# Kernel optimization log

Hardware: AMD Instinct MI355X
Metric: run time of the kernel (lower is better)

## Reference

```python
import jax, jax.numpy as jnp
import numpy as np

N_EMBD = 768
N_HEAD = 12
N_KV_HEAD = 4                      # repeat factor in _repeat_kv
NUM_KV_HEADS = N_HEAD // N_KV_HEAD # 3 actual kv heads
HEAD_DIM = N_EMBD // N_HEAD        # 64
BLOCK_SIZE = 1024                  # sliding window size
SCALE = (HEAD_DIM * N_KV_HEAD / N_HEAD) ** (-0.5)


def _rotary_cos_sin(T, d, dtype):
    inv_freq = 1.0 / (10000.0 ** (jnp.arange(0, d, 2, dtype=jnp.float32) / d))
    t = jnp.arange(T, dtype=jnp.float32)
    freqs = jnp.outer(t, inv_freq)  # (T, d/2)
    return jnp.cos(freqs).astype(dtype)[None, None], jnp.sin(freqs).astype(dtype)[None, None]


def _apply_rotary(x):
    # x: (b, h, T, d)
    T, d = x.shape[2], x.shape[3]
    cos, sin = _rotary_cos_sin(T, d, x.dtype)
    x1, x2 = x[..., : d // 2], x[..., d // 2 :]
    return jnp.concatenate([x1 * cos - x2 * sin, x1 * sin + x2 * cos], axis=-1)


def setup_inputs() -> dict:
    key = jax.random.key(0)
    k0, k1, k2, k3, k4 = jax.random.split(key, 5)
    b, T = 2, 2048
    s = 0.02
    return {
        "hidden_states": jax.random.normal(k0, (b, T, N_EMBD), jnp.float32),
        "Wq": jax.random.normal(k1, (N_HEAD * HEAD_DIM, N_EMBD), jnp.float32) * s,
        "Wk": jax.random.normal(k2, (NUM_KV_HEADS * HEAD_DIM, N_EMBD), jnp.float32) * s,
        "Wv": jax.random.normal(k3, (NUM_KV_HEADS * HEAD_DIM, N_EMBD), jnp.float32) * s,
        "Wo": jax.random.normal(k4, (N_EMBD, N_HEAD * HEAD_DIM), jnp.float32) * s,
    }


def reference(hidden_states, Wq, Wk, Wv, Wo):
    b, T, _ = hidden_states.shape
    q = (hidden_states @ Wq.T).reshape(b, T, N_HEAD, HEAD_DIM).transpose(0, 2, 1, 3)
    k = (hidden_states @ Wk.T).reshape(b, T, NUM_KV_HEADS, HEAD_DIM).transpose(0, 2, 1, 3)
    v = (hidden_states @ Wv.T).reshape(b, T, NUM_KV_HEADS, HEAD_DIM).transpose(0, 2, 1, 3)

    # _repeat_kv: each kv head repeated n_kv_head (=4) times contiguously
    k = jnp.repeat(k, N_KV_HEAD, axis=1)
    v = jnp.repeat(v, N_KV_HEAD, axis=1)

    q = _apply_rotary(q)
    k = _apply_rotary(k)

    # centered sliding-window mask (faithful to per-token loop):
    # window_start = clip(i - W//2, 0, T - W); window is always exactly W wide
    W = BLOCK_SIZE
    i = jnp.arange(T)[:, None]
    j = jnp.arange(T)[None, :]
    start = jnp.clip(i - W // 2, 0, T - W)
    mask = (j >= start) & (j < start + W)  # (T, T)

    scores = jnp.einsum("bhqd,bhkd->bhqk", q, k) * SCALE
    scores = jnp.where(mask[None, None], scores, jnp.finfo(scores.dtype).min)
    attn = jax.nn.softmax(scores, axis=-1)
    out = jnp.einsum("bhqk,bhkd->bhqd", attn, v)  # (b, h, T, d)

    out = out.transpose(0, 2, 1, 3).reshape(b, T, N_EMBD)
    return out @ Wo.T
```

## Files before the change

kernel.cpp:

```cpp
#include <hip/hip_runtime.h>
#include <math.h>

#define T_SEQ 2048
#define E 768
#define WIN 1024
#define KDIM 768
#define HS_SZ ((size_t)4096 * 768)
#define SCALE 0.21650635094610965f

typedef _Float16 f16x8 __attribute__((ext_vector_type(8)));
typedef _Float16 f16x4 __attribute__((ext_vector_type(4)));
typedef float f32x4 __attribute__((ext_vector_type(4)));
typedef __attribute__((address_space(3))) _Float16 lf16;

#define MFMA16(a, b, c) __builtin_amdgcn_mfma_f32_16x16x32_f16(a, b, c, 0, 0, 0)

__device__ __forceinline__ void dma16(const _Float16* g, lf16* l) {
    __builtin_amdgcn_global_load_lds(
        (const __attribute__((address_space(1))) void*)g,
        (__attribute__((address_space(3))) void*)l, 16, 0, 0);
}

__device__ __forceinline__ void cast8(const float* __restrict__ src,
                                      _Float16* __restrict__ dst, int i) {
    float4 a = *(const float4*)&src[i];
    float4 b = *(const float4*)&src[i + 4];
    f16x8 h;
    h[0] = (_Float16)a.x; h[1] = (_Float16)a.y; h[2] = (_Float16)a.z; h[3] = (_Float16)a.w;
    h[4] = (_Float16)b.x; h[5] = (_Float16)b.y; h[6] = (_Float16)b.z; h[7] = (_Float16)b.w;
    *(f16x8*)&dst[i] = h;
}

__global__ __launch_bounds__(256) void prep(
    const float* __restrict__ hs,
    const float* __restrict__ Wq, const float* __restrict__ Wk,
    const float* __restrict__ Wv, const float* __restrict__ Wo,
    _Float16* __restrict__ hs16,
    _Float16* __restrict__ Wq16, _Float16* __restrict__ Wk16,
    _Float16* __restrict__ Wv16, _Float16* __restrict__ Wo16,
    float2* __restrict__ rtab) {
    int tid = blockIdx.x * 256 + threadIdx.x;
    int i = tid * 8;
    if (i < 768 * 768) { cast8(Wq, Wq16, i); cast8(Wo, Wo16, i); }
    if (i < 192 * 768) { cast8(Wk, Wk16, i); cast8(Wv, Wv16, i); }
    cast8(hs, hs16, i);
    if (tid < 2048 * 32) {
        int t = tid >> 5, d = tid & 31;
        float inv = powf(10000.0f, -(float)(2 * d) * (1.0f / 64.0f));
        float s, c;
        sincosf((float)t * inv, &s, &c);
        rtab[tid] = make_float2(c, s);
    }
}

__global__ __launch_bounds__(256) void gemm_qkv(
    const _Float16* __restrict__ A16,
    const _Float16* __restrict__ Wq16, const _Float16* __restrict__ Wk16,
    const _Float16* __restrict__ Wv16, const float2* __restrict__ rtab,
    _Float16* __restrict__ q16, _Float16* __restrict__ k16,
    _Float16* __restrict__ vT16) {
    __shared__ __align__(16) _Float16 As[128 * 128];
    __shared__ __align__(16) _Float16 Bs[64 * 128];
    const int tid = threadIdx.x;
    const int bx = blockIdx.x;
    const int m0 = blockIdx.y * 128;
    const int w = tid >> 6, lane = tid & 63;
    const int mm = lane & 15, quad = lane >> 4;

    const _Float16* bbase; int brb;
    if (bx < 12)      { bbase = Wq16; brb = bx * 64; }
    else if (bx < 15) { bbase = Wk16; brb = (bx - 12) * 64; }
    else              { bbase = Wv16; brb = (bx - 15) * 64; }

    const int rofs4 = lane >> 4;
    const int gs = lane & 15;

    const _Float16* agp[8]; lf16* alp[8];
    #pragma unroll
    for (int j = 0; j < 8; ++j) {
        int c = j * 4 + w;
        int rr = c * 4 + rofs4;
        int glog = gs ^ (rr & 15);
        agp[j] = A16 + (size_t)(m0 + rr) * KDIM + glog * 8;
        alp[j] = ((lf16*)As) + c * 512 + lane * 8;
    }
    const _Float16* bgp[4]; lf16* blp[4];
    #pragma unroll
    for (int j = 0; j < 4; ++j) {
        int c = j * 4 + w;
        int rr = c * 4 + rofs4;
        int glog = gs ^ (rr & 15);
        bgp[j] = bbase + (size_t)(brb + rr) * KDIM + glog * 8;
        blp[j] = ((lf16*)Bs) + c * 512 + lane * 8;
    }

    f32x4 acc[2][4] = {};

    for (int it = 0; it < 6; ++it) {
        const int ke = it * 128;
        __syncthreads();
        #pragma unroll
        for (int j = 0; j < 8; ++j) dma16(agp[j] + ke, alp[j]);
        #pragma unroll
        for (int j = 0; j < 4; ++j) dma16(bgp[j] + ke, blp[j]);
        __syncthreads();
        #pragma unroll
        for (int s = 0; s < 4; ++s) {
            const int gq = ((s * 4 + quad) ^ mm) * 8;
            f16x8 ah[2];
            #pragma unroll
            for (int mt = 0; mt < 2; ++mt)
                ah[mt] = *(const f16x8*)&As[(w * 32 + mt * 16 + mm) * 128 + gq];
            #pragma unroll
            for (int nt = 0; nt < 4; ++nt) {
                f16x8 bh = *(const f16x8*)&Bs[(nt * 16 + mm) * 128 + gq];
                #pragma unroll
                for (int mt = 0; mt < 2; ++mt)
                    acc[mt][nt] = MFMA16(ah[mt], bh, acc[mt][nt]);
            }
        }
    }

    #pragma unroll
    for (int mt = 0; mt < 2; ++mt) {
        #pragma unroll
        for (int r = 0; r < 4; ++r) {
            int row = m0 + w * 32 + mt * 16 + quad * 4 + r;
            int t = row & (T_SEQ - 1);
            int b = row >> 11;
            if (bx < 12) {
                _Float16* dst = &q16[(size_t)row * E + bx * 64 + mm];
                #pragma unroll
                for (int nt = 0; nt < 2; ++nt) {
                    int d = nt * 16 + mm;
                    float2 cs = rtab[t * 32 + d];
                    float x1 = acc[mt][nt][r], x2 = acc[mt][nt + 2][r];
                    dst[nt * 16]       = (_Float16)((x1 * cs.x - x2 * cs.y) * SCALE);
                    dst[(nt + 2) * 16] = (_Float16)((x1 * cs.y + x2 * cs.x) * SCALE);
                }
            } else if (bx < 15) {
                int kvh = bx - 12;
                _Float16* dst = &k16[(((size_t)(b * 3 + kvh)) * T_SEQ + t) * 64 + mm];
                #pragma unroll
                for (int nt = 0; nt < 2; ++nt) {
                    int d = nt * 16 + mm;
                    float2 cs = rtab[t * 32 + d];
                    float x1 = acc[mt][nt][r], x2 = acc[mt][nt + 2][r];
                    dst[nt * 16]       = (_Float16)(x1 * cs.x - x2 * cs.y);
                    dst[(nt + 2) * 16] = (_Float16)(x1 * cs.y + x2 * cs.x);
                }
            } else {
                int kvh = bx - 15;
                #pragma unroll
                for (int nt = 0; nt < 4; ++nt) {
                    int d = nt * 16 + mm;
                    vT16[(((size_t)(b * 3 + kvh)) * 64 + d) * T_SEQ + t] = (_Float16)acc[mt][nt][r];
                }
            }
        }
    }
}

__global__ __launch_bounds__(256) void gemm_out(
    const _Float16* __restrict__ A16, const _Float16* __restrict__ B16,
    float* __restrict__ C) {
    __shared__ __align__(16) _Float16 As[64 * 128];
    __shared__ __align__(16) _Float16 Bs[64 * 128];
    const int tid = threadIdx.x;
    const int n0 = blockIdx.x * 64;
    const int m0 = blockIdx.y * 64;
    const int w = tid >> 6, lane = tid & 63;
    const int mm = lane & 15, quad = lane >> 4;
    const int wm = (w & 1) * 32, wn = (w >> 1) * 32;

    const int rofs4 = lane >> 4;
    const int gs = lane & 15;

    const _Float16* agp[4]; lf16* alp[4];
    const _Float16* bgp[4]; lf16* blp[4];
    #pragma unroll
    for (int j = 0; j < 4; ++j) {
        int c = j * 4 + w;
        int rr = c * 4 + rofs4;
        int glog = gs ^ (rr & 15);
        agp[j] = A16 + (size_t)(m0 + rr) * KDIM + glog * 8;
        alp[j] = ((lf16*)As) + c * 512 + lane * 8;
        bgp[j] = B16 + (size_t)(n0 + rr) * KDIM + glog * 8;
        blp[j] = ((lf16*)Bs) + c * 512 + lane * 8;
    }

    f32x4 acc[2][2] = {};

    for (int it = 0; it < 6; ++it) {
        const int ke = it * 128;
        __syncthreads();
        #pragma unroll
        for (int j = 0; j < 4; ++j) dma16(agp[j] + ke, alp[j]);
        #pragma unroll
        for (int j = 0; j < 4; ++j) dma16(bgp[j] + ke, blp[j]);
        __syncthreads();
        #pragma unroll
        for (int s = 0; s < 4; ++s) {
            const int gq = ((s * 4 + quad) ^ mm) * 8;
            f16x8 ah[2], bh[2];
            #pragma unroll
            for (int mt = 0; mt < 2; ++mt)
                ah[mt] = *(const f16x8*)&As[(wm + mt * 16 + mm) * 128 + gq];
            #pragma unroll
            for (int nt = 0; nt < 2; ++nt)
                bh[nt] = *(const f16x8*)&Bs[(wn + nt * 16 + mm) * 128 + gq];
            #pragma unroll
            for (int nt = 0; nt < 2; ++nt)
                #pragma unroll
                for (int mt = 0; mt < 2; ++mt)
                    acc[mt][nt] = MFMA16(ah[mt], bh[nt], acc[mt][nt]);
        }
    }
    #pragma unroll
    for (int mt = 0; mt < 2; ++mt)
        #pragma unroll
        for (int r = 0; r < 4; ++r) {
            int row = m0 + wm + mt * 16 + quad * 4 + r;
            float* cp = &C[(size_t)row * 768 + n0 + wn + mm];
            #pragma unroll
            for (int nt = 0; nt < 2; ++nt)
                cp[nt * 16] = acc[mt][nt][r];
        }
}

__global__ __launch_bounds__(256) void attn_mfma(const _Float16* __restrict__ q16,
                                                 const _Float16* __restrict__ k16,
                                                 const _Float16* __restrict__ vT16,
                                                 _Float16* __restrict__ aout16) {
    __shared__ __align__(16) char smem[8192 + 8192 + 10240];
    _Float16* k_s  = (_Float16*)smem;
    _Float16* vT_s = (_Float16*)(smem + 8192);
    _Float16 (*p_s)[40] = (_Float16(*)[40])(smem + 16384);
    float* ored = (float*)smem;
    float* lred = (float*)(smem + 16384);

    const int b = blockIdx.z, h = blockIdx.y;
    const int i0 = blockIdx.x * 64;
    const int plane = b * 3 + (h >> 2);
    const int tid = threadIdx.x;
    const int w = tid >> 6, lane = tid & 63;
    const int m = lane & 15, quad = lane >> 4;
    const int qh = w & 1, kh = w >> 1;
    const int xm = m & 7;

    int s0 = i0 - 512;      s0 = s0 < 0 ? 0 : (s0 > 1024 ? 1024 : s0);
    int sL = i0 + 63 - 512; sL = sL < 0 ? 0 : (sL > 1024 ? 1024 : sL);
    const int nc = (sL + WIN - s0 + 63) >> 6;

    int start_q[2];
    f16x8 qf[2][2];
    #pragma unroll
    for (int qt = 0; qt < 2; ++qt) {
        int qi = i0 + qh * 32 + qt * 16 + m;
        int sq = qi - 512; sq = sq < 0 ? 0 : (sq > 1024 ? 1024 : sq);
        start_q[qt] = sq;
        const _Float16* qp = &q16[((size_t)(b * T_SEQ + qi)) * E + h * 64 + quad * 8];
        qf[qt][0] = *(const f16x8*)&qp[0];
        qf[qt][1] = *(const f16x8*)&qp[32];
    }

    f32x4 o[2][4] = {};
    float l_run[2] = {0.0f, 0.0f};

    const int rofs = lane >> 3;
    const int glog = (lane & 7) ^ rofs;
    const _Float16* kgb[2]; const _Float16* vgb[2];
    _Float16* klw[2]; _Float16* vlw[2];
    #pragma unroll
    for (int j = 0; j < 2; ++j) {
        int rr = (j * 4 + w) * 8 + rofs;
        kgb[j] = k16 + ((size_t)plane * T_SEQ + rr) * 64 + glog * 8;
        vgb[j] = vT16 + ((size_t)plane * 64 + rr) * T_SEQ + glog * 8;
        klw[j] = k_s + (j * 4 + w) * 512 + lane * 8;
        vlw[j] = vT_s + (j * 4 + w) * 512 + lane * 8;
    }

    f16x8 kr[2], vr[2];
    #pragma unroll
    for (int j = 0; j < 2; ++j) {
        kr[j] = *(const f16x8*)(kgb[j] + (size_t)s0 * 64);
        vr[j] = *(const f16x8*)(vgb[j] + s0);
    }

    for (int ci = 0; ci < nc; ++ci) {
        const int c0 = s0 + ci * 64;
        __syncthreads();
        #pragma unroll
        for (int j = 0; j < 2; ++j) {
            *(f16x8*)klw[j] = kr[j];
            *(f16x8*)vlw[j] = vr[j];
        }
        __syncthreads();
        if (ci + 1 < nc) {
            const int cn = c0 + 64;
            #pragma unroll
            for (int j = 0; j < 2; ++j) {
                kr[j] = *(const f16x8*)(kgb[j] + (size_t)cn * 64);
                vr[j] = *(const f16x8*)(vgb[j] + cn);
            }
        }

        f32x4 st[2][2] = {};
        #pragma unroll
        for (int s = 0; s < 2; ++s) {
            #pragma unroll
            for (int kt = 0; kt < 2; ++kt) {
                int row = kh * 32 + kt * 16 + m;
                int g = (s * 4 + quad) ^ xm;
                f16x8 a = *(const f16x8*)&k_s[row * 64 + g * 8];
                #pragma unroll
                for (int qt = 0; qt < 2; ++qt)
                    st[kt][qt] = MFMA16(a, qf[qt][s], st[kt][qt]);
            }
        }

        const bool boundary = (c0 < sL) || (c0 + 63 > s0 + 1023);
        if (boundary) {
            #pragma unroll
            for (int kt = 0; kt < 2; ++kt)
                #pragma unroll
                for (int qt = 0; qt < 2; ++qt)
                    #pragma unroll
                    for (int r = 0; r < 4; ++r) {
                        int j = c0 + kh * 32 + kt * 16 + quad * 4 + r;
                        bool valid = (j >= start_q[qt]) && (j < start_q[qt] + WIN);
                        st[kt][qt][r] = valid ? st[kt][qt][r] : -INFINITY;
                    }
        }

        #pragma unroll
        for (int kt = 0; kt < 2; ++kt)
            #pragma unroll
            for (int qt = 0; qt < 2; ++qt) {
                float p0 = __expf(st[kt][qt][0]);
                float p1 = __expf(st[kt][qt][1]);
                float p2 = __expf(st[kt][qt][2]);
                float p3 = __expf(st[kt][qt][3]);
                l_run[qt] += (p0 + p1) + (p2 + p3);
                f16x4 pv = {(_Float16)p0, (_Float16)p1, (_Float16)p2, (_Float16)p3};
                *(f16x4*)&p_s[w * 32 + qt * 16 + m][kt * 16 + quad * 4] = pv;
            }

        f16x8 bp[2];
        #pragma unroll
        for (int qt = 0; qt < 2; ++qt)
            bp[qt] = *(const f16x8*)&p_s[w * 32 + qt * 16 + m][quad * 8];
        #pragma unroll
        for (int mt = 0; mt < 4; ++mt) {
            int g = (kh * 4 + quad) ^ xm;
            f16x8 a = *(const f16x8*)&vT_s[(mt * 16 + m) * 64 + g * 8];
            #pragma unroll
            for (int qt = 0; qt < 2; ++qt)
                o[qt][mt] = MFMA16(a, bp[qt], o[qt][mt]);
        }
    }

    float l_tot[2];
    #pragma unroll
    for (int qt = 0; qt < 2; ++qt) {
        float l = l_run[qt];
        l += __shfl_xor(l, 16);
        l += __shfl_xor(l, 32);
        l_tot[qt] = l;
    }

    __syncthreads();
    if (kh == 1) {
        #pragma unroll
        for (int qt = 0; qt < 2; ++qt) {
            #pragma unroll
            for (int mt = 0; mt < 4; ++mt) {
                int idx = ((qh * 32 + qt * 16 + m) << 6) + mt * 16 + quad * 4;
                *(float4*)&ored[idx] = *(float4*)&o[qt][mt];
            }
            if (quad == 0) lred[qh * 32 + qt * 16 + m] = l_tot[qt];
        }
    }
    __syncthreads();
    if (kh == 0) {
        #pragma unroll
        for (int qt = 0; qt < 2; ++qt) {
            float rl = 1.0f / (l_tot[qt] + lred[qh * 32 + qt * 16 + m]);
            int qi = i0 + qh * 32 + qt * 16 + m;
            _Float16* op = &aout16[((size_t)(b * T_SEQ + qi)) * E + h * 64];
            #pragma unroll
            for (int mt = 0; mt < 4; ++mt) {
                int idx = ((qh * 32 + qt * 16 + m) << 6) + mt * 16 + quad * 4;
                float4 other = *(float4*)&ored[idx];
                #pragma unroll
                for (int r = 0; r < 4; ++r) {
                    float x = (o[qt][mt][r] + (&other.x)[r]) * rl;
                    op[mt * 16 + quad * 4 + r] = (_Float16)x;
                }
            }
        }
    }
}

extern "C" void kernel_launch(void* const* d_in, const int* in_sizes, int n_in,
                              void* d_out, int out_size, void* d_ws, size_t ws_size,
                              hipStream_t stream) {
    const float* hs = (const float*)d_in[0];
    const float* Wq = (const float*)d_in[1];
    const float* Wk = (const float*)d_in[2];
    const float* Wv = (const float*)d_in[3];
    const float* Wo = (const float*)d_in[4];
    float* out = (float*)d_out;

    _Float16* hs16   = (_Float16*)d_ws;
    _Float16* aout16 = hs16 + HS_SZ;
    _Float16* q16    = aout16 + HS_SZ;
    _Float16* k16    = q16 + HS_SZ;
    _Float16* vT16   = k16 + 6 * 2048 * 64;
    _Float16* Wq16   = vT16 + 6 * 2048 * 64;
    _Float16* Wk16   = Wq16 + 768 * 768;
    _Float16* Wv16   = Wk16 + 192 * 768;
    _Float16* Wo16   = Wv16 + 192 * 768;
    float2*   rtab   = (float2*)(Wo16 + 768 * 768);

    dim3 blk(256);
    prep<<<dim3((int)(HS_SZ / 8 / 256)), blk, 0, stream>>>(hs, Wq, Wk, Wv, Wo,
                                                           hs16, Wq16, Wk16, Wv16, Wo16, rtab);
    gemm_qkv<<<dim3(18, 32), blk, 0, stream>>>(hs16, Wq16, Wk16, Wv16, rtab, q16, k16, vT16);
    attn_mfma<<<dim3(32, 12, 2), blk, 0, stream>>>(q16, k16, vT16, aout16);
    gemm_out<<<dim3(12, 64), blk, 0, stream>>>(aout16, Wo16, out);
}
```

Baseline: 135.2 us.

## Stage V transpose through LDS, double-buffer attention K/V, enlarge output GEMM tile

The V-projection epilogue now writes its tile into shared memory and emits coalesced 16-byte rows of vT, replacing scattered 2-byte strided stores. The attention kernel double-buffers its K/V shared tiles, which removes one barrier per chunk, and writes its output as 4-wide half vectors. The output GEMM uses 128-row tiles with a 4-wide N loop per wave, halving the grid for more reuse of the Wo tile. Costs are more shared memory in attention, which may lower occupancy, and fewer output GEMM blocks.

```diff
diff --git a/kernel.cpp b/kernel.cpp
--- a/kernel.cpp
+++ b/kernel.cpp
@@ -121,14 +121,13 @@
         }
     }
 
-    #pragma unroll
-    for (int mt = 0; mt < 2; ++mt) {
-        #pragma unroll
-        for (int r = 0; r < 4; ++r) {
-            int row = m0 + w * 32 + mt * 16 + quad * 4 + r;
-            int t = row & (T_SEQ - 1);
-            int b = row >> 11;
-            if (bx < 12) {
+    if (bx < 12) {
+        #pragma unroll
+        for (int mt = 0; mt < 2; ++mt)
+            #pragma unroll
+            for (int r = 0; r < 4; ++r) {
+                int row = m0 + w * 32 + mt * 16 + quad * 4 + r;
+                int t = row & (T_SEQ - 1);
                 _Float16* dst = &q16[(size_t)row * E + bx * 64 + mm];
                 #pragma unroll
                 for (int nt = 0; nt < 2; ++nt) {
@@ -138,8 +137,16 @@
                     dst[nt * 16]       = (_Float16)((x1 * cs.x - x2 * cs.y) * SCALE);
                     dst[(nt + 2) * 16] = (_Float16)((x1 * cs.y + x2 * cs.x) * SCALE);
                 }
-            } else if (bx < 15) {
-                int kvh = bx - 12;
+            }
+    } else if (bx < 15) {
+        int kvh = bx - 12;
+        #pragma unroll
+        for (int mt = 0; mt < 2; ++mt)
+            #pragma unroll
+            for (int r = 0; r < 4; ++r) {
+                int row = m0 + w * 32 + mt * 16 + quad * 4 + r;
+                int t = row & (T_SEQ - 1);
+                int b = row >> 11;
                 _Float16* dst = &k16[(((size_t)(b * 3 + kvh)) * T_SEQ + t) * 64 + mm];
                 #pragma unroll
                 for (int nt = 0; nt < 2; ++nt) {
@@ -149,14 +156,28 @@
                     dst[nt * 16]       = (_Float16)(x1 * cs.x - x2 * cs.y);
                     dst[(nt + 2) * 16] = (_Float16)(x1 * cs.y + x2 * cs.x);
                 }
-            } else {
-                int kvh = bx - 15;
-                #pragma unroll
-                for (int nt = 0; nt < 4; ++nt) {
-                    int d = nt * 16 + mm;
-                    vT16[(((size_t)(b * 3 + kvh)) * 64 + d) * T_SEQ + t] = (_Float16)acc[mt][nt][r];
-                }
-            }
+            }
+    } else {
+        __syncthreads();
+        _Float16 (*vs)[136] = (_Float16 (*)[136])As;
+        #pragma unroll
+        for (int mt = 0; mt < 2; ++mt)
+            #pragma unroll
+            for (int nt = 0; nt < 4; ++nt) {
+                f16x4 pv;
+                #pragma unroll
+                for (int r = 0; r < 4; ++r) pv[r] = (_Float16)acc[mt][nt][r];
+                *(f16x4*)&vs[nt * 16 + mm][w * 32 + mt * 16 + quad * 4] = pv;
+            }
+        __syncthreads();
+        const int kvh = bx - 15;
+        const int b = m0 >> 11, tbase = m0 & (T_SEQ - 1);
+        const int tl = (tid & 15) * 8;
+        #pragma unroll
+        for (int j = 0; j < 4; ++j) {
+            int dd = (tid >> 4) + j * 16;
+            f16x8 vv = *(const f16x8*)&vs[dd][tl];
+            *(f16x8*)&vT16[(((size_t)(b * 3 + kvh)) * 64 + dd) * T_SEQ + tbase + tl] = vv;
         }
     }
 }
@@ -164,66 +185,71 @@
 __global__ __launch_bounds__(256) void gemm_out(
     const _Float16* __restrict__ A16, const _Float16* __restrict__ B16,
     float* __restrict__ C) {
-    __shared__ __align__(16) _Float16 As[64 * 128];
+    __shared__ __align__(16) _Float16 As[128 * 128];
     __shared__ __align__(16) _Float16 Bs[64 * 128];
     const int tid = threadIdx.x;
     const int n0 = blockIdx.x * 64;
-    const int m0 = blockIdx.y * 64;
+    const int m0 = blockIdx.y * 128;
     const int w = tid >> 6, lane = tid & 63;
     const int mm = lane & 15, quad = lane >> 4;
-    const int wm = (w & 1) * 32, wn = (w >> 1) * 32;
 
     const int rofs4 = lane >> 4;
     const int gs = lane & 15;
 
-    const _Float16* agp[4]; lf16* alp[4];
-    const _Float16* bgp[4]; lf16* blp[4];
-    #pragma unroll
-    for (int j = 0; j < 4; ++j) {
+    const _Float16* agp[8]; lf16* alp[8];
+    #pragma unroll
+    for (int j = 0; j < 8; ++j) {
         int c = j * 4 + w;
         int rr = c * 4 + rofs4;
         int glog = gs ^ (rr & 15);
         agp[j] = A16 + (size_t)(m0 + rr) * KDIM + glog * 8;
         alp[j] = ((lf16*)As) + c * 512 + lane * 8;
+    }
+    const _Float16* bgp[4]; lf16* blp[4];
+    #pragma unroll
+    for (int j = 0; j < 4; ++j) {
+        int c = j * 4 + w;
+        int rr = c * 4 + rofs4;
+        int glog = gs ^ (rr & 15);
         bgp[j] = B16 + (size_t)(n0 + rr) * KDIM + glog * 8;
         blp[j] = ((lf16*)Bs) + c * 512 + lane * 8;
     }
 
-    f32x4 acc[2][2] = {};
+    f32x4 acc[2][4] = {};
 
     for (int it = 0; it < 6; ++it) {
         const int ke = it * 128;
         __syncthreads();
         #pragma unroll
-        for (int j = 0; j < 4; ++j) dma16(agp[j] + ke, alp[j]);
+        for (int j = 0; j < 8; ++j) dma16(agp[j] + ke, alp[j]);
         #pragma unroll
         for (int j = 0; j < 4; ++j) dma16(bgp[j] + ke, blp[j]);
         __syncthreads();
         #pragma unroll
         for (int s = 0; s < 4; ++s) {
             const int gq = ((s * 4 + quad) ^ mm) * 8;
-            f16x8 ah[2], bh[2];
+            f16x8 ah[2];
             #pragma unroll
             for (int mt = 0; mt < 2; ++mt)
-                ah[mt] = *(const f16x8*)&As[(wm + mt * 16 + mm) * 128 + gq];
-            #pragma unroll
-            for (int nt = 0; nt < 2; ++nt)
-                bh[nt] = *(const f16x8*)&Bs[(wn + nt * 16 + mm) * 128 + gq];
-            #pragma unroll
-            for (int nt = 0; nt < 2; ++nt)
+                ah[mt] = *(const f16x8*)&As[(w * 32 + mt * 16 + mm) * 128 + gq];
+            #pragma unroll
+            for (int nt = 0; nt < 4; ++nt) {
+                f16x8 bh = *(const f16x8*)&Bs[(nt * 16 + mm) * 128 + gq];
                 #pragma unroll
                 for (int mt = 0; mt < 2; ++mt)
-                    acc[mt][nt] = MFMA16(ah[mt], bh[nt], acc[mt][nt]);
-        }
-    }
+                    acc[mt][nt] = MFMA16(ah[mt], bh, acc[mt][nt]);
+            }
+        }
+    }
+
     #pragma unroll
     for (int mt = 0; mt < 2; ++mt)
         #pragma unroll
         for (int r = 0; r < 4; ++r) {
-            int row = m0 + wm + mt * 16 + quad * 4 + r;
-            float* cp = &C[(size_t)row * 768 + n0 + wn + mm];
-            #pragma unroll
-            for (int nt = 0; nt < 2; ++nt)
+            int row = m0 + w * 32 + mt * 16 + quad * 4 + r;
+            float* cp = &C[(size_t)row * 768 + n0 + mm];
+            #pragma unroll
+            for (int nt = 0; nt < 4; ++nt)
                 cp[nt * 16] = acc[mt][nt][r];
         }
 }
@@ -232,10 +258,10 @@
                                                  const _Float16* __restrict__ k16,
                                                  const _Float16* __restrict__ vT16,
                                                  _Float16* __restrict__ aout16) {
-    __shared__ __align__(16) char smem[8192 + 8192 + 10240];
+    __shared__ __align__(16) char smem[32768 + 10240];
     _Float16* k_s  = (_Float16*)smem;
-    _Float16* vT_s = (_Float16*)(smem + 8192);
-    _Float16 (*p_s)[40] = (_Float16(*)[40])(smem + 16384);
+    _Float16* vT_s = (_Float16*)(smem + 16384);
+    _Float16 (*p_s)[40] = (_Float16(*)[40])(smem + 32768);
     float* ored = (float*)smem;
     float* lred = (float*)(smem + 16384);
 
@@ -286,15 +312,15 @@
         kr[j] = *(const f16x8*)(kgb[j] + (size_t)s0 * 64);
         vr[j] = *(const f16x8*)(vgb[j] + s0);
     }
+    #pragma unroll
+    for (int j = 0; j < 2; ++j) {
+        *(f16x8*)klw[j] = kr[j];
+        *(f16x8*)vlw[j] = vr[j];
+    }
 
     for (int ci = 0; ci < nc; ++ci) {
         const int c0 = s0 + ci * 64;
-        __syncthreads();
-        #pragma unroll
-        for (int j = 0; j < 2; ++j) {
-            *(f16x8*)klw[j] = kr[j];
-            *(f16x8*)vlw[j] = vr[j];
-        }
+        const int sel = (ci & 1) * 4096;
         __syncthreads();
         if (ci + 1 < nc) {
             const int cn = c0 + 64;
@@ -312,7 +338,7 @@
             for (int kt = 0; kt < 2; ++kt) {
                 int row = kh * 32 + kt * 16 + m;
                 int g = (s * 4 + quad) ^ xm;
-                f16x8 a = *(const f16x8*)&k_s[row * 64 + g * 8];
+                f16x8 a = *(const f16x8*)&k_s[sel + row * 64 + g * 8];
                 #pragma unroll
                 for (int qt = 0; qt < 2; ++qt)
                     st[kt][qt] = MFMA16(a, qf[qt][s], st[kt][qt]);
@@ -353,10 +379,19 @@
         #pragma unroll
         for (int mt = 0; mt < 4; ++mt) {
             int g = (kh * 4 + quad) ^ xm;
-            f16x8 a = *(const f16x8*)&vT_s[(mt * 16 + m) * 64 + g * 8];
+            f16x8 a = *(const f16x8*)&vT_s[sel + (mt * 16 + m) * 64 + g * 8];
             #pragma unroll
             for (int qt = 0; qt < 2; ++qt)
                 o[qt][mt] = MFMA16(a, bp[qt], o[qt][mt]);
+        }
+
+        if (ci + 1 < nc) {
+            const int ns = ((ci + 1) & 1) * 4096;
+            #pragma unroll
+            for (int j = 0; j < 2; ++j) {
+                *(f16x8*)(klw[j] + ns) = kr[j];
+                *(f16x8*)(vlw[j] + ns) = vr[j];
+            }
         }
     }
 
@@ -392,11 +427,11 @@
             for (int mt = 0; mt < 4; ++mt) {
                 int idx = ((qh * 32 + qt * 16 + m) << 6) + mt * 16 + quad * 4;
                 float4 other = *(float4*)&ored[idx];
-                #pragma unroll
-                for (int r = 0; r < 4; ++r) {
-                    float x = (o[qt][mt][r] + (&other.x)[r]) * rl;
-                    op[mt * 16 + quad * 4 + r] = (_Float16)x;
-                }
+                f16x4 hv;
+                #pragma unroll
+                for (int r = 0; r < 4; ++r)
+                    hv[r] = (_Float16)((o[qt][mt][r] + (&other.x)[r]) * rl);
+                *(f16x4*)&op[mt * 16 + quad * 4] = hv;
             }
         }
     }
@@ -428,5 +463,5 @@
                                                            hs16, Wq16, Wk16, Wv16, Wo16, rtab);
     gemm_qkv<<<dim3(18, 32), blk, 0, stream>>>(hs16, Wq16, Wk16, Wv16, rtab, q16, k16, vT16);
     attn_mfma<<<dim3(32, 12, 2), blk, 0, stream>>>(q16, k16, vT16, aout16);
-    gemm_out<<<dim3(12, 64), blk, 0, stream>>>(aout16, Wo16, out);
-}
+    gemm_out<<<dim3(12, 32), blk, 0, stream>>>(aout16, Wo16, out);
+}
```

Result: no change. 133.2 us (-1.5%).
